# Performance work log

Measured on AMD Instinct MI355X. Metric: run time of the kernel, lower is better.

Reference implementation:

```python
import jax, jax.numpy as jnp
import numpy as np

L, D, H, DFF, V, NB = 8, 1024, 16, 4096, 50257, 2048
HD = D // H
B, T = 2, 2048
EPS = 1e-5


def setup_inputs() -> dict:
    key = jax.random.key(0)
    ks = jax.random.split(key, 10)
    s = 0.02
    return {
        "x": jax.random.randint(ks[0], (B, T), 0, V),
        "W_emb": jax.random.normal(ks[1], (V, D), jnp.float32) * s,  # tied tok_emb / out_head
        "pos_emb": jax.random.normal(ks[2], (NB, D), jnp.float32) * s,
        "Wq": jax.random.normal(ks[3], (L, D, D), jnp.float32) * s,
        "Wk": jax.random.normal(ks[4], (L, D, D), jnp.float32) * s,
        "Wv": jax.random.normal(ks[5], (L, D, D), jnp.float32) * s,
        "Wo": jax.random.normal(ks[6], (L, D, D), jnp.float32) * s,
        "bo": jnp.zeros((L, D), jnp.float32),
        "n1_scale": jnp.ones((L, D), jnp.float32),
        "n1_shift": jnp.zeros((L, D), jnp.float32),
        "n2_scale": jnp.ones((L, D), jnp.float32),
        "n2_shift": jnp.zeros((L, D), jnp.float32),
        "W1": jax.random.normal(ks[7], (L, DFF, D), jnp.float32) * s,
        "b1": jnp.zeros((L, DFF), jnp.float32),
        "W2": jax.random.normal(ks[8], (L, D, DFF), jnp.float32) * s,
        "b2": jnp.zeros((L, D), jnp.float32),
        "f_scale": jnp.ones((D,), jnp.float32),
        "f_shift": jnp.zeros((D,), jnp.float32),
    }


def layernorm(x, scale, shift):
    # Matches custom LayerNorm: uses sample std (ddof=1) and (std + eps) in denominator
    mean = jnp.mean(x, axis=-1, keepdims=True)
    std = jnp.std(x, axis=-1, keepdims=True, ddof=1)
    return scale * ((x - mean) / (std + EPS)) + shift


def gelu(x):
    c = jnp.sqrt(jnp.asarray(2.0 / jnp.pi, x.dtype))
    return 0.5 * x * (1.0 + jnp.tanh(c * (x + 0.044715 * x * x * x)))


def reference(x, W_emb, pos_emb, Wq, Wk, Wv, Wo, bo,
              n1_scale, n1_shift, n2_scale, n2_shift,
              W1, b1, W2, b2, f_scale, f_shift):
    b, t = x.shape
    h = W_emb[x] + pos_emb[:t]  # [B,T,D]
    causal = jnp.triu(jnp.ones((t, t), dtype=bool), 1)  # True above diagonal => masked
    scale = jnp.sqrt(jnp.asarray(HD, h.dtype))
    neg_inf = jnp.asarray(-jnp.inf, h.dtype)
    for l in range(L):
        xn = layernorm(h, n1_scale[l], n1_shift[l])
        q = (xn @ Wq[l].T).reshape(b, t, H, HD).transpose(0, 2, 1, 3)  # [B,H,T,hd]
        k = (xn @ Wk[l].T).reshape(b, t, H, HD).transpose(0, 2, 1, 3)
        v = (xn @ Wv[l].T).reshape(b, t, H, HD).transpose(0, 2, 1, 3)
        scores = jnp.einsum('bhqd,bhkd->bhqk', q, k)
        scores = jnp.where(causal, neg_inf, scores) / scale  # mask then scale, as in source
        aw = jax.nn.softmax(scores, axis=-1)
        ctx = jnp.einsum('bhqk,bhkd->bhqd', aw, v)
        ctx = ctx.transpose(0, 2, 1, 3).reshape(b, t, D)
        h = h + (ctx @ Wo[l].T + bo[l])
        xn2 = layernorm(h, n2_scale[l], n2_shift[l])
        h = h + (gelu(xn2 @ W1[l].T + b1[l]) @ W2[l].T + b2[l])
    h = layernorm(h, f_scale, f_shift)
    logits = h[:, -1:, :] @ W_emb.T  # last-token logits [B,1,V] (targets=None path)
    return logits
```

## Files before the change

### kernel.cpp

```cpp
#include <hip/hip_runtime.h>
#include <math.h>

#define L_   8
#define D_   1024
#define H_   16
#define HD_  64
#define DFF_ 4096
#define V_   50257
#define T_   2048
#define B_   2
#define M_   (B_*T_)

typedef __attribute__((ext_vector_type(8))) short short8;
typedef __attribute__((ext_vector_type(4))) float f4;
typedef __attribute__((ext_vector_type(4))) unsigned short us4;

#define GLOAD16(gp, lp) \
  __builtin_amdgcn_global_load_lds((__attribute__((address_space(1))) void*)(gp), \
                                   (__attribute__((address_space(3))) void*)(lp), 16, 0, 0)

__device__ __forceinline__ unsigned short f2bf(float f) {
  union { float f; unsigned u; } c; c.f = f;
  return (unsigned short)((c.u + 0x7fffu + ((c.u >> 16) & 1u)) >> 16);
}

__global__ __launch_bounds__(256) void cvt_kernel(const float* __restrict__ s,
                                                  unsigned short* __restrict__ d, int n) {
  int i = (blockIdx.x * 256 + threadIdx.x) * 4;
  const int stride = gridDim.x * 256 * 4;
  for (; i < n; i += stride) {
    f4 f = *(const f4*)(s + i);
    us4 o;
    o.x = f2bf(f.x); o.y = f2bf(f.y); o.z = f2bf(f.z); o.w = f2bf(f.w);
    *(us4*)(d + i) = o;
  }
}

__global__ __launch_bounds__(256) void embed_kernel(const int* __restrict__ x,
    const float* __restrict__ wemb, const float* __restrict__ pos, float* __restrict__ h) {
  const int m = blockIdx.x;
  const int t = m & (T_ - 1);
  const int idx = x[m];
  const int d = threadIdx.x * 4;
  f4 a = *(const f4*)(wemb + (size_t)idx * D_ + d);
  f4 b = *(const f4*)(pos + (size_t)t * D_ + d);
  a = a + b;
  *(f4*)(h + (size_t)m * D_ + d) = a;
}

__global__ __launch_bounds__(256) void ln_kernel(const float* __restrict__ h,
    const float* __restrict__ sc, const float* __restrict__ sh,
    unsigned short* __restrict__ out) {
  const int row = blockIdx.x, tid = threadIdx.x;
  f4 x = *(const f4*)(h + (size_t)row * D_ + tid * 4);
  float s1 = x.x + x.y + x.z + x.w;
  float s2 = x.x * x.x + x.y * x.y + x.z * x.z + x.w * x.w;
#pragma unroll
  for (int off = 32; off > 0; off >>= 1) {
    s1 += __shfl_down(s1, off);
    s2 += __shfl_down(s2, off);
  }
  __shared__ float r1[4], r2[4];
  if ((tid & 63) == 0) { r1[tid >> 6] = s1; r2[tid >> 6] = s2; }
  __syncthreads();
  float t1 = r1[0] + r1[1] + r1[2] + r1[3];
  float t2 = r2[0] + r2[1] + r2[2] + r2[3];
  float mean = t1 * (1.0f / D_);
  float var = fmaxf((t2 - t1 * mean) * (1.0f / (D_ - 1)), 0.0f);
  float inv = 1.0f / (sqrtf(var) + 1e-5f);
  f4 s = *(const f4*)(sc + tid * 4);
  f4 b = *(const f4*)(sh + tid * 4);
  us4 o;
  o.x = f2bf(s.x * ((x.x - mean) * inv) + b.x);
  o.y = f2bf(s.y * ((x.y - mean) * inv) + b.y);
  o.z = f2bf(s.z * ((x.z - mean) * inv) + b.z);
  o.w = f2bf(s.w * ((x.w - mean) * inv) + b.w);
  *(us4*)(out + (size_t)row * D_ + tid * 4) = o;
}

__global__ __launch_bounds__(256) void ln_final_kernel(const float* __restrict__ h,
    const float* __restrict__ sc, const float* __restrict__ sh, float* __restrict__ out) {
  const int b = blockIdx.x, tid = threadIdx.x;
  const int row = b * T_ + (T_ - 1);
  f4 x = *(const f4*)(h + (size_t)row * D_ + tid * 4);
  float s1 = x.x + x.y + x.z + x.w;
  float s2 = x.x * x.x + x.y * x.y + x.z * x.z + x.w * x.w;
#pragma unroll
  for (int off = 32; off > 0; off >>= 1) {
    s1 += __shfl_down(s1, off);
    s2 += __shfl_down(s2, off);
  }
  __shared__ float r1[4], r2[4];
  if ((tid & 63) == 0) { r1[tid >> 6] = s1; r2[tid >> 6] = s2; }
  __syncthreads();
  float t1 = r1[0] + r1[1] + r1[2] + r1[3];
  float t2 = r2[0] + r2[1] + r2[2] + r2[3];
  float mean = t1 * (1.0f / D_);
  float var = fmaxf((t2 - t1 * mean) * (1.0f / (D_ - 1)), 0.0f);
  float inv = 1.0f / (sqrtf(var) + 1e-5f);
  f4 s = *(const f4*)(sc + tid * 4);
  f4 bb = *(const f4*)(sh + tid * 4);
  f4 o;
  o.x = s.x * ((x.x - mean) * inv) + bb.x;
  o.y = s.y * ((x.y - mean) * inv) + bb.y;
  o.z = s.z * ((x.z - mean) * inv) + bb.z;
  o.w = s.w * ((x.w - mean) * inv) + bb.w;
  *(f4*)(out + (size_t)b * D_ + tid * 4) = o;
}

#define EP_QKV 0
#define EP_RES 1
#define EP_GELU 2

template <int MODE>
__global__ __launch_bounds__(256) void gemm_kernel(
    const unsigned short* __restrict__ A,
    const unsigned short* __restrict__ Bq,
    const unsigned short* __restrict__ Bk,
    const unsigned short* __restrict__ Bv,
    const float* __restrict__ bias,
    float* __restrict__ hres,
    unsigned short* __restrict__ out0,
    unsigned short* __restrict__ out1,
    unsigned short* __restrict__ out2,
    int N, int K) {
  __shared__ __attribute__((aligned(16))) unsigned short As[128 * 32];
  __shared__ __attribute__((aligned(16))) unsigned short Bs[128 * 32];
  const int tid = threadIdx.x;
  const int wv = tid >> 6, lane = tid & 63;
  const int quad = lane >> 4, l16 = lane & 15;
  const int bm0 = blockIdx.x * 128;
  int bn0;
  const unsigned short* Bw;
  unsigned short* qout = out0;
  if (MODE == EP_QKV) {
    int sel = blockIdx.y >> 3;
    bn0 = (blockIdx.y & 7) * 128;
    Bw = (sel == 0) ? Bq : ((sel == 1) ? Bk : Bv);
    qout = (sel == 0) ? out0 : ((sel == 1) ? out1 : out2);
  } else {
    bn0 = blockIdx.y * 128;
    Bw = Bq;
  }
  const int wm = (wv & 1) * 64, wn = (wv >> 1) * 64;

  f4 acc[4][4] = {};

  for (int k0 = 0; k0 < K; k0 += 32) {
#pragma unroll
    for (int i = 0; i < 2; i++) {
      int c = i * 256 + tid;
      int row = c >> 2;
      int c4 = (c & 3) ^ (row & 3);
      GLOAD16(A + (size_t)(bm0 + row) * K + k0 + c4 * 8,
              (char*)As + (i * 256 + wv * 64) * 16);
      GLOAD16(Bw + (size_t)(bn0 + row) * K + k0 + c4 * 8,
              (char*)Bs + (i * 256 + wv * 64) * 16);
    }
    __syncthreads();
    short8 af[4], bfr[4];
#pragma unroll
    for (int mt = 0; mt < 4; mt++) {
      int row = wm + mt * 16 + l16;
      af[mt] = *(const short8*)(As + row * 32 + ((quad ^ (row & 3)) * 8));
    }
#pragma unroll
    for (int nt = 0; nt < 4; nt++) {
      int row = wn + nt * 16 + l16;
      bfr[nt] = *(const short8*)(Bs + row * 32 + ((quad ^ (row & 3)) * 8));
    }
#pragma unroll
    for (int mt = 0; mt < 4; mt++)
#pragma unroll
      for (int nt = 0; nt < 4; nt++)
        acc[mt][nt] = __builtin_amdgcn_mfma_f32_16x16x32_bf16(af[mt], bfr[nt], acc[mt][nt], 0, 0, 0);
    __syncthreads();
  }

#pragma unroll
  for (int mt = 0; mt < 4; mt++) {
#pragma unroll
    for (int nt = 0; nt < 4; nt++) {
#pragma unroll
      for (int r = 0; r < 4; r++) {
        int gm = bm0 + wm + mt * 16 + quad * 4 + r;
        int gn = bn0 + wn + nt * 16 + l16;
        float val = acc[mt][nt][r];
        if (MODE == EP_QKV) {
          int b = gm >> 11, t = gm & (T_ - 1);
          int hh = gn >> 6, hd = gn & 63;
          qout[(size_t)((b * H_ + hh) * T_ + t) * HD_ + hd] = f2bf(val);
        } else if (MODE == EP_RES) {
          size_t idx = (size_t)gm * D_ + gn;
          hres[idx] += val + bias[gn];
        } else {
          float xg = val + bias[gn];
          float z = 0.7978845608028654f * (xg + 0.044715f * xg * xg * xg);
          float e = __expf(2.0f * z);
          float th = 1.0f - 2.0f / (e + 1.0f);
          out0[(size_t)gm * DFF_ + gn] = f2bf(0.5f * xg * (1.0f + th));
        }
      }
    }
  }
}

__global__ __launch_bounds__(256) void vtrans_kernel(const unsigned short* __restrict__ v,
                                                     unsigned short* __restrict__ vt) {
  __shared__ __attribute__((aligned(16))) unsigned short tile[64 * 72];
  const int tid = threadIdx.x;
  const int t0 = blockIdx.x * 64;
  const size_t bh = (size_t)(blockIdx.z * H_ + blockIdx.y);
  const unsigned short* vp = v + bh * T_ * HD_;
#pragma unroll
  for (int i = 0; i < 2; i++) {
    int c = i * 256 + tid;
    int row = c >> 3, c8 = c & 7;
    *(short8*)(tile + row * 72 + c8 * 8) =
        *(const short8*)(vp + (size_t)(t0 + row) * HD_ + c8 * 8);
  }
  __syncthreads();
  unsigned short* op = vt + bh * (size_t)HD_ * T_;
#pragma unroll
  for (int i = 0; i < 2; i++) {
    int c = i * 256 + tid;
    int drow = c >> 3, c8 = c & 7;
    short8 o;
#pragma unroll
    for (int j = 0; j < 8; j++) o[j] = (short)tile[(c8 * 8 + j) * 72 + drow];
    *(short8*)(op + (size_t)drow * T_ + t0 + c8 * 8) = o;
  }
}

#define ATTN_STEP(QF0, QF1, OF, MR, LR, QT)                                        \
  {                                                                                \
    float sv[4][4];                                                                \
    _Pragma("unroll") for (int nt = 0; nt < 4; nt++) {                             \
      int row = nt * 16 + l16;                                                     \
      int p0 = (quad ^ (row & 7)) * 8;                                             \
      int p1 = ((4 + quad) ^ (row & 7)) * 8;                                       \
      short8 kf0 = *(const short8*)(Ks + row * 64 + p0);                           \
      short8 kf1 = *(const short8*)(Ks + row * 64 + p1);                           \
      f4 z = {};                                                                   \
      z = __builtin_amdgcn_mfma_f32_16x16x32_bf16(QF0, kf0, z, 0, 0, 0);           \
      z = __builtin_amdgcn_mfma_f32_16x16x32_bf16(QF1, kf1, z, 0, 0, 0);           \
      _Pragma("unroll") for (int r = 0; r < 4; r++) {                              \
        float s = z[r] * 0.125f;                                                   \
        if (kt == (QT)) {                                                          \
          int col = kb + nt * 16 + l16;                                            \
          int rowg = (QT) * 64 + wv * 16 + quad * 4 + r;                           \
          if (col > rowg) s = -1e30f;                                              \
        }                                                                          \
        sv[nt][r] = s;                                                             \
      }                                                                            \
    }                                                                              \
    float mnew[4], alpha[4];                                                       \
    _Pragma("unroll") for (int r = 0; r < 4; r++) {                                \
      float mx = fmaxf(fmaxf(sv[0][r], sv[1][r]), fmaxf(sv[2][r], sv[3][r]));      \
      mx = fmaxf(mx, __shfl_xor(mx, 1));                                           \
      mx = fmaxf(mx, __shfl_xor(mx, 2));                                           \
      mx = fmaxf(mx, __shfl_xor(mx, 4));                                           \
      mx = fmaxf(mx, __shfl_xor(mx, 8));                                           \
      mnew[r] = fmaxf(MR[r], mx);                                                  \
      alpha[r] = __expf(MR[r] - mnew[r]);                                          \
      MR[r] = mnew[r];                                                             \
    }                                                                              \
    float pv[4][4];                                                                \
    _Pragma("unroll") for (int nt = 0; nt < 4; nt++)                               \
      _Pragma("unroll") for (int r = 0; r < 4; r++)                                \
        pv[nt][r] = __expf(sv[nt][r] - mnew[r]);                                   \
    _Pragma("unroll") for (int r = 0; r < 4; r++) {                                \
      float s = pv[0][r] + pv[1][r] + pv[2][r] + pv[3][r];                         \
      s += __shfl_xor(s, 1);                                                       \
      s += __shfl_xor(s, 2);                                                       \
      s += __shfl_xor(s, 4);                                                       \
      s += __shfl_xor(s, 8);                                                       \
      LR[r] = LR[r] * alpha[r] + s;                                                \
    }                                                                              \
    _Pragma("unroll") for (int nt = 0; nt < 4; nt++) {                             \
      OF[nt][0] *= alpha[0];                                                       \
      OF[nt][1] *= alpha[1];                                                       \
      OF[nt][2] *= alpha[2];                                                       \
      OF[nt][3] *= alpha[3];                                                       \
    }                                                                              \
    _Pragma("unroll") for (int nt = 0; nt < 4; nt++)                               \
      _Pragma("unroll") for (int r = 0; r < 4; r++)                                \
        pw[(quad * 4 + r) * 88 + nt * 16 + l16] = f2bf(pv[nt][r]);                 \
    short8 pf0 = *(const short8*)(pw + l16 * 88 + quad * 8);                       \
    short8 pf1 = *(const short8*)(pw + l16 * 88 + 32 + quad * 8);                  \
    _Pragma("unroll") for (int nt = 0; nt < 4; nt++) {                             \
      int row = nt * 16 + l16;                                                     \
      int p0 = (quad ^ (row & 7)) * 8;                                             \
      int p1 = ((4 + quad) ^ (row & 7)) * 8;                                       \
      short8 vf0 = *(const short8*)(Vs + row * 64 + p0);                           \
      short8 vf1 = *(const short8*)(Vs + row * 64 + p1);                           \
      OF[nt] = __builtin_amdgcn_mfma_f32_16x16x32_bf16(pf0, vf0, OF[nt], 0, 0, 0); \
      OF[nt] = __builtin_amdgcn_mfma_f32_16x16x32_bf16(pf1, vf1, OF[nt], 0, 0, 0); \
    }                                                                              \
  }

__global__ __launch_bounds__(256, 2) void attn_kernel(
    const unsigned short* __restrict__ q,
    const unsigned short* __restrict__ k,
    const unsigned short* __restrict__ vt,
    unsigned short* __restrict__ ctx) {
  __shared__ __attribute__((aligned(16))) unsigned short Ks[64 * 64];
  __shared__ __attribute__((aligned(16))) unsigned short Vs[64 * 64];
  __shared__ __attribute__((aligned(16))) unsigned short Ps[4][16 * 88];
  const int tid = threadIdx.x;
  const int wv = tid >> 6, lane = tid & 63;
  const int quad = lane >> 4, l16 = lane & 15;
  const int bx = blockIdx.x, hh = blockIdx.y, b = blockIdx.z;
  const int qtA = bx, qtB = 31 - bx;
  const size_t bh = (size_t)(b * H_ + hh);
  const unsigned short* qp = q + bh * T_ * HD_;
  const unsigned short* kp = k + bh * T_ * HD_;
  const unsigned short* vp = vt + bh * (size_t)HD_ * T_;

  const int qrA = qtA * 64 + wv * 16 + l16;
  const int qrB = qtB * 64 + wv * 16 + l16;
  const short8 qfA0 = *(const short8*)(qp + (size_t)qrA * HD_ + quad * 8);
  const short8 qfA1 = *(const short8*)(qp + (size_t)qrA * HD_ + 32 + quad * 8);
  const short8 qfB0 = *(const short8*)(qp + (size_t)qrB * HD_ + quad * 8);
  const short8 qfB1 = *(const short8*)(qp + (size_t)qrB * HD_ + 32 + quad * 8);

  f4 ofA[4] = {}, ofB[4] = {};
  float mA[4] = {-1e30f, -1e30f, -1e30f, -1e30f}, lA[4] = {0.f, 0.f, 0.f, 0.f};
  float mB[4] = {-1e30f, -1e30f, -1e30f, -1e30f}, lB[4] = {0.f, 0.f, 0.f, 0.f};
  unsigned short* pw = Ps[wv];

  const int nkt = qtB + 1;
  for (int kt = 0; kt < nkt; kt++) {
    const int kb = kt * 64;
#pragma unroll
    for (int i = 0; i < 2; i++) {
      int c = i * 256 + tid;
      int row = c >> 3;
      int c8 = (c & 7) ^ (row & 7);
      GLOAD16(kp + (size_t)(kb + row) * HD_ + c8 * 8, (char*)Ks + (i * 256 + wv * 64) * 16);
      GLOAD16(vp + (size_t)row * T_ + kb + c8 * 8, (char*)Vs + (i * 256 + wv * 64) * 16);
    }
    __syncthreads();
    ATTN_STEP(qfB0, qfB1, ofB, mB, lB, qtB);
    if (kt <= qtA) ATTN_STEP(qfA0, qfA1, ofA, mA, lA, qtA);
    __syncthreads();
  }
#pragma unroll
  for (int nt = 0; nt < 4; nt++) {
#pragma unroll
    for (int r = 0; r < 4; r++) {
      int dcol = hh * HD_ + nt * 16 + l16;
      int rowgB = qtB * 64 + wv * 16 + quad * 4 + r;
      ctx[(size_t)(b * T_ + rowgB) * D_ + dcol] = f2bf(ofB[nt][r] / lB[r]);
      int rowgA = qtA * 64 + wv * 16 + quad * 4 + r;
      ctx[(size_t)(b * T_ + rowgA) * D_ + dcol] = f2bf(ofA[nt][r] / lA[r]);
    }
  }
}

__global__ __launch_bounds__(256) void logits_kernel(const float* __restrict__ wemb,
    const float* __restrict__ hln, float* __restrict__ out) {
  const int tid = threadIdx.x;
  const int wv = tid >> 6, lane = tid & 63;
  const int rbase = blockIdx.x * 32 + wv * 8;
  f4 h0[4], h1[4];
#pragma unroll
  for (int j = 0; j < 4; j++) {
    h0[j] = *(const f4*)(hln + j * 256 + lane * 4);
    h1[j] = *(const f4*)(hln + D_ + j * 256 + lane * 4);
  }
#pragma unroll
  for (int i = 0; i < 8; i++) {
    int r = rbase + i;
    if (r >= V_) return;
    const float* wr = wemb + (size_t)r * D_;
    float a0 = 0.f, a1 = 0.f;
#pragma unroll
    for (int j = 0; j < 4; j++) {
      f4 w4 = *(const f4*)(wr + j * 256 + lane * 4);
      a0 += w4.x * h0[j].x + w4.y * h0[j].y + w4.z * h0[j].z + w4.w * h0[j].w;
      a1 += w4.x * h1[j].x + w4.y * h1[j].y + w4.z * h1[j].z + w4.w * h1[j].w;
    }
#pragma unroll
    for (int off = 32; off > 0; off >>= 1) {
      a0 += __shfl_down(a0, off);
      a1 += __shfl_down(a1, off);
    }
    if (lane == 0) {
      out[r] = a0;
      out[V_ + r] = a1;
    }
  }
}

extern "C" void kernel_launch(void* const* d_in, const int* in_sizes, int n_in,
                              void* d_out, int out_size, void* d_ws, size_t ws_size,
                              hipStream_t stream) {
  (void)in_sizes; (void)n_in; (void)out_size; (void)ws_size;
  const int*   x    = (const int*)  d_in[0];
  const float* Wemb = (const float*)d_in[1];
  const float* pos  = (const float*)d_in[2];
  const float* Wq   = (const float*)d_in[3];
  const float* Wk   = (const float*)d_in[4];
  const float* Wv   = (const float*)d_in[5];
  const float* Wo   = (const float*)d_in[6];
  const float* bo   = (const float*)d_in[7];
  const float* n1s  = (const float*)d_in[8];
  const float* n1b  = (const float*)d_in[9];
  const float* n2s  = (const float*)d_in[10];
  const float* n2b  = (const float*)d_in[11];
  const float* W1   = (const float*)d_in[12];
  const float* b1   = (const float*)d_in[13];
  const float* W2   = (const float*)d_in[14];
  const float* b2   = (const float*)d_in[15];
  const float* fsc  = (const float*)d_in[16];
  const float* fsh  = (const float*)d_in[17];
  float* out = (float*)d_out;

  char* p = (char*)d_ws;
  auto alloc = [&](size_t bytes) -> char* {
    char* r = p;
    p += (bytes + 255) & ~(size_t)255;
    return r;
  };
  unsigned short* wq_b = (unsigned short*)alloc((size_t)L_ * D_ * D_ * 2);
  unsigned short* wk_b = (unsigned short*)alloc((size_t)L_ * D_ * D_ * 2);
  unsigned short* wv_b = (unsigned short*)alloc((size_t)L_ * D_ * D_ * 2);
  unsigned short* wo_b = (unsigned short*)alloc((size_t)L_ * D_ * D_ * 2);
  unsigned short* w1_b = (unsigned short*)alloc((size_t)L_ * DFF_ * D_ * 2);
  unsigned short* w2_b = (unsigned short*)alloc((size_t)L_ * DFF_ * D_ * 2);
  float*          h    = (float*)alloc((size_t)M_ * D_ * 4);
  unsigned short* xn   = (unsigned short*)alloc((size_t)M_ * D_ * 2);
  unsigned short* qb   = (unsigned short*)alloc((size_t)M_ * D_ * 2);
  unsigned short* kb   = (unsigned short*)alloc((size_t)M_ * D_ * 2);
  unsigned short* vb   = (unsigned short*)alloc((size_t)M_ * D_ * 2);
  unsigned short* vtb  = (unsigned short*)alloc((size_t)M_ * D_ * 2);
  unsigned short* ctx  = (unsigned short*)alloc((size_t)M_ * D_ * 2);
  unsigned short* act  = (unsigned short*)alloc((size_t)M_ * DFF_ * 2);
  float*          hln  = (float*)alloc(2 * D_ * 4);

  cvt_kernel<<<2048, 256, 0, stream>>>(Wq, wq_b, L_ * D_ * D_);
  cvt_kernel<<<2048, 256, 0, stream>>>(Wk, wk_b, L_ * D_ * D_);
  cvt_kernel<<<2048, 256, 0, stream>>>(Wv, wv_b, L_ * D_ * D_);
  cvt_kernel<<<2048, 256, 0, stream>>>(Wo, wo_b, L_ * D_ * D_);
  cvt_kernel<<<2048, 256, 0, stream>>>(W1, w1_b, L_ * DFF_ * D_);
  cvt_kernel<<<2048, 256, 0, stream>>>(W2, w2_b, L_ * DFF_ * D_);
  embed_kernel<<<M_, 256, 0, stream>>>(x, Wemb, pos, h);

  for (int l = 0; l < L_; l++) {
    ln_kernel<<<M_, 256, 0, stream>>>(h, n1s + l * D_, n1b + l * D_, xn);
    gemm_kernel<EP_QKV><<<dim3(32, 24), 256, 0, stream>>>(
        xn, wq_b + (size_t)l * D_ * D_, wk_b + (size_t)l * D_ * D_,
        wv_b + (size_t)l * D_ * D_, nullptr, nullptr, qb, kb, vb, D_, D_);
    vtrans_kernel<<<dim3(32, H_, B_), 256, 0, stream>>>(vb, vtb);
    attn_kernel<<<dim3(16, H_, B_), 256, 0, stream>>>(qb, kb, vtb, ctx);
    gemm_kernel<EP_RES><<<dim3(32, 8), 256, 0, stream>>>(
        ctx, wo_b + (size_t)l * D_ * D_, nullptr, nullptr,
        bo + l * D_, h, nullptr, nullptr, nullptr, D_, D_);
    ln_kernel<<<M_, 256, 0, stream>>>(h, n2s + l * D_, n2b + l * D_, xn);
    gemm_kernel<EP_GELU><<<dim3(32, 32), 256, 0, stream>>>(
        xn, w1_b + (size_t)l * DFF_ * D_, nullptr, nullptr,
        b1 + l * DFF_, nullptr, act, nullptr, nullptr, DFF_, D_);
    gemm_kernel<EP_RES><<<dim3(32, 8), 256, 0, stream>>>(
        act, w2_b + (size_t)l * DFF_ * D_, nullptr, nullptr,
        b2 + l * D_, h, nullptr, nullptr, nullptr, D_, DFF_);
  }
  ln_final_kernel<<<2, 256, 0, stream>>>(h, fsc, fsh, hln);
  logits_kernel<<<(V_ + 31) / 32, 256, 0, stream>>>(Wemb, hln, out);
}
```

Baseline: 3.263 ms.

## Double-buffer GEMM LDS tiles with K-step 64 and prefetch next tile

The bf16 MFMA GEMM kernel now keeps two LDS buffers per operand and doubles the K tile from 32 to 64, with a wider XOR swizzle to match. The next tile's global-to-LDS loads are issued before the current tile's MFMAs, and each iteration ends with one barrier instead of two. This is meant to hide global load latency behind matrix math and cut barrier overhead. In exchange, LDS use rises to 64KB per block, and launch bounds now request 2 blocks per CU, which may constrain register allocation.

```diff
diff --git a/kernel.cpp b/kernel.cpp
--- a/kernel.cpp
+++ b/kernel.cpp
@@ -113,7 +113,7 @@
 #define EP_GELU 2
 
 template <int MODE>
-__global__ __launch_bounds__(256) void gemm_kernel(
+__global__ __launch_bounds__(256, 2) void gemm_kernel(
     const unsigned short* __restrict__ A,
     const unsigned short* __restrict__ Bq,
     const unsigned short* __restrict__ Bk,
@@ -124,8 +124,8 @@
     unsigned short* __restrict__ out1,
     unsigned short* __restrict__ out2,
     int N, int K) {
-  __shared__ __attribute__((aligned(16))) unsigned short As[128 * 32];
-  __shared__ __attribute__((aligned(16))) unsigned short Bs[128 * 32];
+  __shared__ __attribute__((aligned(16))) unsigned short As[2][128 * 64];
+  __shared__ __attribute__((aligned(16))) unsigned short Bs[2][128 * 64];
   const int tid = threadIdx.x;
   const int wv = tid >> 6, lane = tid & 63;
   const int quad = lane >> 4, l16 = lane & 15;
@@ -146,35 +146,48 @@
 
   f4 acc[4][4] = {};
 
-  for (int k0 = 0; k0 < K; k0 += 32) {
-#pragma unroll
-    for (int i = 0; i < 2; i++) {
+  const int nkt = K >> 6;
+
+  auto STAGE = [&](int buf, int t) {
+    const int k0 = t << 6;
+#pragma unroll
+    for (int i = 0; i < 4; i++) {
       int c = i * 256 + tid;
-      int row = c >> 2;
-      int c4 = (c & 3) ^ (row & 3);
-      GLOAD16(A + (size_t)(bm0 + row) * K + k0 + c4 * 8,
-              (char*)As + (i * 256 + wv * 64) * 16);
-      GLOAD16(Bw + (size_t)(bn0 + row) * K + k0 + c4 * 8,
-              (char*)Bs + (i * 256 + wv * 64) * 16);
+      int row = c >> 3;
+      int c8 = (c & 7) ^ (row & 7);
+      GLOAD16(A + (size_t)(bm0 + row) * K + k0 + c8 * 8,
+              (char*)As[buf] + (i * 256 + wv * 64) * 16);
+      GLOAD16(Bw + (size_t)(bn0 + row) * K + k0 + c8 * 8,
+              (char*)Bs[buf] + (i * 256 + wv * 64) * 16);
+    }
+  };
+
+  STAGE(0, 0);
+  __syncthreads();
+  int cur = 0;
+  for (int t = 0; t < nkt; t++) {
+    if (t + 1 < nkt) STAGE(cur ^ 1, t + 1);
+#pragma unroll
+    for (int ks = 0; ks < 2; ks++) {
+      short8 af[4], bfr[4];
+#pragma unroll
+      for (int mt = 0; mt < 4; mt++) {
+        int row = wm + mt * 16 + l16;
+        af[mt] = *(const short8*)(As[cur] + row * 64 + (((ks * 4 + quad) ^ (row & 7)) * 8));
+      }
+#pragma unroll
+      for (int nt = 0; nt < 4; nt++) {
+        int row = wn + nt * 16 + l16;
+        bfr[nt] = *(const short8*)(Bs[cur] + row * 64 + (((ks * 4 + quad) ^ (row & 7)) * 8));
+      }
+#pragma unroll
+      for (int mt = 0; mt < 4; mt++)
+#pragma unroll
+        for (int nt = 0; nt < 4; nt++)
+          acc[mt][nt] = __builtin_amdgcn_mfma_f32_16x16x32_bf16(af[mt], bfr[nt], acc[mt][nt], 0, 0, 0);
     }
     __syncthreads();
-    short8 af[4], bfr[4];
-#pragma unroll
-    for (int mt = 0; mt < 4; mt++) {
-      int row = wm + mt * 16 + l16;
-      af[mt] = *(const short8*)(As + row * 32 + ((quad ^ (row & 3)) * 8));
-    }
-#pragma unroll
-    for (int nt = 0; nt < 4; nt++) {
-      int row = wn + nt * 16 + l16;
-      bfr[nt] = *(const short8*)(Bs + row * 32 + ((quad ^ (row & 3)) * 8));
-    }
-#pragma unroll
-    for (int mt = 0; mt < 4; mt++)
-#pragma unroll
-      for (int nt = 0; nt < 4; nt++)
-        acc[mt][nt] = __builtin_amdgcn_mfma_f32_16x16x32_bf16(af[mt], bfr[nt], acc[mt][nt], 0, 0, 0);
-    __syncthreads();
+    cur ^= 1;
   }
 
 #pragma unroll
```

Result: faster. 3.037 ms (-6.9%).
